# Kernel tuning notes

Measured on AMD Instinct MI355X. Metric: run time of the kernel, lower is better.

The kernel has to match this reference:

```python
import jax, jax.numpy as jnp
import numpy as np

D_MODEL = 1024
N_HEAD = 16
D_K = D_MODEL // N_HEAD
FFN = 4096
EPS = 1e-5


def layer_norm(x, g, b):
    mu = jnp.mean(x, axis=-1, keepdims=True)
    var = jnp.var(x, axis=-1, keepdims=True)
    return (x - mu) * jax.lax.rsqrt(var + EPS) * g + b


def setup_inputs() -> dict:
    key = jax.random.key(0)
    ks = jax.random.split(key, 16)
    B, L = 2, 2048
    s = 1.0 / np.sqrt(D_MODEL)
    inp = {
        "x": jax.random.normal(ks[0], (B, L, D_MODEL), dtype=jnp.float32),
        "mask": jnp.ones((B, 1, 1, L), dtype=jnp.int32),
        "ln1_g": jnp.ones((D_MODEL,), jnp.float32),
        "ln1_b": jnp.zeros((D_MODEL,), jnp.float32),
        "Wq": jax.random.normal(ks[1], (D_MODEL, D_MODEL), jnp.float32) * s,
        "bq": jnp.zeros((D_MODEL,), jnp.float32),
        "Wk": jax.random.normal(ks[2], (D_MODEL, D_MODEL), jnp.float32) * s,
        "bk": jnp.zeros((D_MODEL,), jnp.float32),
        "Wv": jax.random.normal(ks[3], (D_MODEL, D_MODEL), jnp.float32) * s,
        "bv": jnp.zeros((D_MODEL,), jnp.float32),
        "Wo": jax.random.normal(ks[4], (D_MODEL, D_MODEL), jnp.float32) * s,
        "bo": jnp.zeros((D_MODEL,), jnp.float32),
        "ln2_g": jnp.ones((D_MODEL,), jnp.float32),
        "ln2_b": jnp.zeros((D_MODEL,), jnp.float32),
        "W1": jax.random.normal(ks[5], (D_MODEL, FFN), jnp.float32) * s,
        "b1": jnp.zeros((FFN,), jnp.float32),
        "W2": jax.random.normal(ks[6], (FFN, D_MODEL), jnp.float32) * (1.0 / np.sqrt(FFN)),
        "b2": jnp.zeros((D_MODEL,), jnp.float32),
    }
    return inp


def reference(x, mask, ln1_g, ln1_b, Wq, bq, Wk, bk, Wv, bv, Wo, bo,
              ln2_g, ln2_b, W1, b1, W2, b2):
    B, L, _ = x.shape
    nx = layer_norm(x, ln1_g, ln1_b)
    # QKV projections, split heads -> [B, H, L, Dk]
    def proj(W, b):
        return (nx @ W + b).reshape(B, L, N_HEAD, D_K).transpose(0, 2, 1, 3)
    q, k, v = proj(Wq, bq), proj(Wk, bk), proj(Wv, bv)
    scores = jnp.einsum('bhqd,bhkd->bhqk', q, k) / np.sqrt(D_K)
    scores = jnp.where(mask.astype(bool), scores, -jnp.inf)
    attn = jax.nn.softmax(scores, axis=-1)
    out = jnp.einsum('bhqk,bhkd->bhqd', attn, v)
    out = out.transpose(0, 2, 1, 3).reshape(B, L, D_MODEL)
    out = out @ Wo + bo
    x = x + out  # residual (dropout p=0)
    nx = layer_norm(x, ln2_g, ln2_b)
    h = jax.nn.silu(nx @ W1 + b1)
    x = x + (h @ W2 + b2)
    return x
```

## Files before the change

### kernel.cpp

```cpp
#include <hip/hip_runtime.h>
#include <hip/hip_bf16.h>

#define D_MODEL 1024
#define N_HEAD  16
#define D_K     64
#define FFN_DIM 4096
#define B_SZ    2
#define L_SEQ   2048
#define ROWS    (B_SZ * L_SEQ)
#define PST     68

typedef float  floatx4 __attribute__((ext_vector_type(4)));
typedef short  shortx8 __attribute__((ext_vector_type(8)));

__device__ __forceinline__ unsigned short f2bf(float f) {
    unsigned int u = __float_as_uint(f);
    unsigned int rounding = 0x7fffu + ((u >> 16) & 1u);
    return (unsigned short)((u + rounding) >> 16);
}
__device__ __forceinline__ float bf2f(unsigned short u) {
    return __uint_as_float(((unsigned int)u) << 16);
}

__device__ __forceinline__ void glds16(const unsigned short* g, unsigned short* l) {
    __builtin_amdgcn_global_load_lds(
        (const __attribute__((address_space(1))) unsigned int*)g,
        (__attribute__((address_space(3))) unsigned int*)l, 16, 0, 0);
}

__global__ __launch_bounds__(256) void ln_kernel(const float* __restrict__ x,
                                                 const float* __restrict__ g,
                                                 const float* __restrict__ b,
                                                 unsigned short* __restrict__ out) {
    const int row = blockIdx.x;
    const int tid = threadIdx.x;
    const float* xr = x + (size_t)row * D_MODEL;
    float4 xv = *reinterpret_cast<const float4*>(&xr[tid * 4]);
    float v[4] = {xv.x, xv.y, xv.z, xv.w};
    float s = v[0] + v[1] + v[2] + v[3];
    float ss = v[0] * v[0] + v[1] * v[1] + v[2] * v[2] + v[3] * v[3];
    __shared__ float r1[256], r2[256];
    r1[tid] = s; r2[tid] = ss;
    __syncthreads();
    for (int off = 128; off > 0; off >>= 1) {
        if (tid < off) { r1[tid] += r1[tid + off]; r2[tid] += r2[tid + off]; }
        __syncthreads();
    }
    const float mean = r1[0] * (1.0f / D_MODEL);
    const float var  = r2[0] * (1.0f / D_MODEL) - mean * mean;
    const float inv  = rsqrtf(var + 1e-5f);
    unsigned short* orow = out + (size_t)row * D_MODEL;
    ushort4 o;
    o.x = f2bf((v[0] - mean) * inv * g[tid * 4 + 0] + b[tid * 4 + 0]);
    o.y = f2bf((v[1] - mean) * inv * g[tid * 4 + 1] + b[tid * 4 + 1]);
    o.z = f2bf((v[2] - mean) * inv * g[tid * 4 + 2] + b[tid * 4 + 2]);
    o.w = f2bf((v[3] - mean) * inv * g[tid * 4 + 3] + b[tid * 4 + 3]);
    *reinterpret_cast<ushort4*>(&orow[tid * 4]) = o;
}

__global__ __launch_bounds__(256) void transpose_cast(const float* __restrict__ W,
                                                      unsigned short* __restrict__ Wt,
                                                      int K, int N) {
    __shared__ unsigned short T[32][33];
    const int t = threadIdx.x;
    const int k0 = blockIdx.y * 32, n0 = blockIdx.x * 32;
    const int kr = t >> 3, nc = (t & 7) * 4;
    float4 w = *reinterpret_cast<const float4*>(&W[(size_t)(k0 + kr) * N + n0 + nc]);
    T[kr][nc + 0] = f2bf(w.x); T[kr][nc + 1] = f2bf(w.y);
    T[kr][nc + 2] = f2bf(w.z); T[kr][nc + 3] = f2bf(w.w);
    __syncthreads();
    const int nr = t >> 3, kc = (t & 7) * 4;
    ushort4 o;
    o.x = T[kc + 0][nr]; o.y = T[kc + 1][nr];
    o.z = T[kc + 2][nr]; o.w = T[kc + 3][nr];
    *reinterpret_cast<ushort4*>(&Wt[(size_t)(n0 + nr) * K + k0 + kc]) = o;
}

__global__ __launch_bounds__(256) void transpose_cast4(const float* s0, const float* s1,
                                                       const float* s2, const float* s3,
                                                       unsigned short* d0, unsigned short* d1,
                                                       unsigned short* d2, unsigned short* d3) {
    const int z = blockIdx.z;
    const float* W = (z == 0) ? s0 : (z == 1) ? s1 : (z == 2) ? s2 : s3;
    unsigned short* Wt = (z == 0) ? d0 : (z == 1) ? d1 : (z == 2) ? d2 : d3;
    __shared__ unsigned short T[32][33];
    const int t = threadIdx.x;
    const int k0 = blockIdx.y * 32, n0 = blockIdx.x * 32;
    const int kr = t >> 3, nc = (t & 7) * 4;
    float4 w = *reinterpret_cast<const float4*>(&W[(size_t)(k0 + kr) * D_MODEL + n0 + nc]);
    T[kr][nc + 0] = f2bf(w.x); T[kr][nc + 1] = f2bf(w.y);
    T[kr][nc + 2] = f2bf(w.z); T[kr][nc + 3] = f2bf(w.w);
    __syncthreads();
    const int nr = t >> 3, kc = (t & 7) * 4;
    ushort4 o;
    o.x = T[kc + 0][nr]; o.y = T[kc + 1][nr];
    o.z = T[kc + 2][nr]; o.w = T[kc + 3][nr];
    *reinterpret_cast<ushort4*>(&Wt[(size_t)(n0 + nr) * D_MODEL + k0 + kc]) = o;
}


template <int SILU, int HAS_RES, int OUT_BF16>
__global__ __launch_bounds__(256) void mfma_gemm(const unsigned short* __restrict__ A,
                                                 const unsigned short* __restrict__ Wt,
                                                 const float* __restrict__ bias,
                                                 const float* __restrict__ res,
                                                 void* __restrict__ outP,
                                                 int M, int N, int K) {
    __shared__ unsigned short As[128 * 32];
    __shared__ unsigned short Bs[128 * 32];
    const int tid  = threadIdx.x;
    const int lane = tid & 63;
    const int wave = tid >> 6;
    const int row0 = blockIdx.y * 128, col0 = blockIdx.x * 128;
    const int wr = (wave >> 1) * 64, wc = (wave & 1) * 64;

    floatx4 acc[4][4] = {};
    const int p0 = tid,       r0s = p0 >> 2, k0s = (((p0 & 3) - (r0s >> 1)) & 3) * 8;
    const int p1 = tid + 256, r1s = p1 >> 2, k1s = (((p1 & 3) - (r1s >> 1)) & 3) * 8;
    const int am = (lane & 15);

    int offA[4], offB[4];
#pragma unroll
    for (int i = 0; i < 4; ++i) {
        const int Ra = wr + i * 16 + am;
        offA[i] = Ra * 32 + (((lane >> 4) + (Ra >> 1)) & 3) * 8;
        const int Rb = wc + i * 16 + am;
        offB[i] = Rb * 32 + (((lane >> 4) + (Rb >> 1)) & 3) * 8;
    }

    for (int kt = 0; kt < K; kt += 32) {
        glds16(A  + (size_t)(row0 + r0s) * K + kt + k0s, &As[p0 * 8]);
        glds16(A  + (size_t)(row0 + r1s) * K + kt + k1s, &As[p1 * 8]);
        glds16(Wt + (size_t)(col0 + r0s) * K + kt + k0s, &Bs[p0 * 8]);
        glds16(Wt + (size_t)(col0 + r1s) * K + kt + k1s, &Bs[p1 * 8]);
        __syncthreads();
        shortx8 af[4], bf[4];
#pragma unroll
        for (int i = 0; i < 4; ++i)
            af[i] = *reinterpret_cast<const shortx8*>(&As[offA[i]]);
#pragma unroll
        for (int j = 0; j < 4; ++j)
            bf[j] = *reinterpret_cast<const shortx8*>(&Bs[offB[j]]);
#pragma unroll
        for (int i = 0; i < 4; ++i)
#pragma unroll
            for (int j = 0; j < 4; ++j)
                acc[i][j] = __builtin_amdgcn_mfma_f32_16x16x32_bf16(af[i], bf[j], acc[i][j], 0, 0, 0);
        __syncthreads();
    }

    const int cq = (lane >> 4) * 4;
    const int cn = lane & 15;
#pragma unroll
    for (int i = 0; i < 4; ++i) {
#pragma unroll
        for (int j = 0; j < 4; ++j) {
            const int n = col0 + wc + j * 16 + cn;
            const float bb = bias[n];
#pragma unroll
            for (int r = 0; r < 4; ++r) {
                const int m = row0 + wr + i * 16 + cq + r;
                float v = acc[i][j][r] + bb;
                if (SILU) v = v / (1.0f + __expf(-v));
                if (HAS_RES) v += res[(size_t)m * N + n];
                if (OUT_BF16) ((unsigned short*)outP)[(size_t)m * N + n] = f2bf(v);
                else          ((float*)outP)[(size_t)m * N + n] = v;
            }
        }
    }
}

__global__ __launch_bounds__(256) void mfma_gemm_qkv(const unsigned short* __restrict__ A,
                                                     const unsigned short* __restrict__ Wt,
                                                     const float* __restrict__ bq,
                                                     const float* __restrict__ bk,
                                                     const float* __restrict__ bv,
                                                     unsigned short* __restrict__ qb,
                                                     unsigned short* __restrict__ kb,
                                                     unsigned short* __restrict__ vtb) {
    const int K = D_MODEL, M = ROWS;
    __shared__ unsigned short As[128 * 32];
    __shared__ unsigned short Bs[128 * 32];
    const int tid  = threadIdx.x;
    const int lane = tid & 63;
    const int wave = tid >> 6;
    const int row0 = blockIdx.y * 128, col0 = blockIdx.x * 128;
    const int wr = (wave >> 1) * 64, wc = (wave & 1) * 64;

    floatx4 acc[4][4] = {};
    const int p0 = tid,       r0s = p0 >> 2, k0s = (((p0 & 3) - (r0s >> 1)) & 3) * 8;
    const int p1 = tid + 256, r1s = p1 >> 2, k1s = (((p1 & 3) - (r1s >> 1)) & 3) * 8;
    const int am = (lane & 15);

    int offA[4], offB[4];
#pragma unroll
    for (int i = 0; i < 4; ++i) {
        const int Ra = wr + i * 16 + am;
        offA[i] = Ra * 32 + (((lane >> 4) + (Ra >> 1)) & 3) * 8;
        const int Rb = wc + i * 16 + am;
        offB[i] = Rb * 32 + (((lane >> 4) + (Rb >> 1)) & 3) * 8;
    }

    for (int kt = 0; kt < K; kt += 32) {
        glds16(A  + (size_t)(row0 + r0s) * K + kt + k0s, &As[p0 * 8]);
        glds16(A  + (size_t)(row0 + r1s) * K + kt + k1s, &As[p1 * 8]);
        glds16(Wt + (size_t)(col0 + r0s) * K + kt + k0s, &Bs[p0 * 8]);
        glds16(Wt + (size_t)(col0 + r1s) * K + kt + k1s, &Bs[p1 * 8]);
        __syncthreads();
        shortx8 af[4], bf[4];
#pragma unroll
        for (int i = 0; i < 4; ++i)
            af[i] = *reinterpret_cast<const shortx8*>(&As[offA[i]]);
#pragma unroll
        for (int j = 0; j < 4; ++j)
            bf[j] = *reinterpret_cast<const shortx8*>(&Bs[offB[j]]);
#pragma unroll
        for (int i = 0; i < 4; ++i)
#pragma unroll
            for (int j = 0; j < 4; ++j)
                acc[i][j] = __builtin_amdgcn_mfma_f32_16x16x32_bf16(af[i], bf[j], acc[i][j], 0, 0, 0);
        __syncthreads();
    }

    const int cq = (lane >> 4) * 4;
    const int cn = lane & 15;
    const int sel = col0 >> 10;
    const int nbase = col0 & 1023;
    const float* bias = (sel == 0) ? bq : (sel == 1) ? bk : bv;
    const float scl = (sel == 0) ? 0.125f : 1.0f;
#pragma unroll
    for (int i = 0; i < 4; ++i) {
#pragma unroll
        for (int j = 0; j < 4; ++j) {
            const int n = nbase + wc + j * 16 + cn;
            const float bb = bias[n];
            if (sel == 2) {
                const int m0 = row0 + wr + i * 16 + cq;
                ushort4 o;
                o.x = f2bf(acc[i][j][0] + bb);
                o.y = f2bf(acc[i][j][1] + bb);
                o.z = f2bf(acc[i][j][2] + bb);
                o.w = f2bf(acc[i][j][3] + bb);
                *reinterpret_cast<ushort4*>(&vtb[(size_t)n * M + m0]) = o;
            } else {
                unsigned short* dst = (sel == 0) ? qb : kb;
#pragma unroll
                for (int r = 0; r < 4; ++r) {
                    const int m = row0 + wr + i * 16 + cq + r;
                    dst[(size_t)m * D_MODEL + n] = f2bf((acc[i][j][r] + bb) * scl);
                }
            }
        }
    }
}

__global__ __launch_bounds__(256) void mfma_gemm_splitk(const unsigned short* __restrict__ A,
                                                        const unsigned short* __restrict__ Wt,
                                                        unsigned short* __restrict__ parts,
                                                        int M, int N, int KS) {
    __shared__ unsigned short As[128 * 32];
    __shared__ unsigned short Bs[128 * 32];
    const int tid  = threadIdx.x;
    const int lane = tid & 63;
    const int wave = tid >> 6;
    const int row0 = blockIdx.y * 128, col0 = blockIdx.x * 128;
    const int wr = (wave >> 1) * 64, wc = (wave & 1) * 64;
    const int K = KS * gridDim.z;
    const int kbeg = blockIdx.z * KS;
    unsigned short* outp = parts + (size_t)blockIdx.z * M * N;

    floatx4 acc[4][4] = {};
    const int p0 = tid,       r0s = p0 >> 2, k0s = (((p0 & 3) - (r0s >> 1)) & 3) * 8;
    const int p1 = tid + 256, r1s = p1 >> 2, k1s = (((p1 & 3) - (r1s >> 1)) & 3) * 8;
    const int am = (lane & 15);

    int offA[4], offB[4];
#pragma unroll
    for (int i = 0; i < 4; ++i) {
        const int Ra = wr + i * 16 + am;
        offA[i] = Ra * 32 + (((lane >> 4) + (Ra >> 1)) & 3) * 8;
        const int Rb = wc + i * 16 + am;
        offB[i] = Rb * 32 + (((lane >> 4) + (Rb >> 1)) & 3) * 8;
    }

    for (int kt = kbeg; kt < kbeg + KS; kt += 32) {
        glds16(A  + (size_t)(row0 + r0s) * K + kt + k0s, &As[p0 * 8]);
        glds16(A  + (size_t)(row0 + r1s) * K + kt + k1s, &As[p1 * 8]);
        glds16(Wt + (size_t)(col0 + r0s) * K + kt + k0s, &Bs[p0 * 8]);
        glds16(Wt + (size_t)(col0 + r1s) * K + kt + k1s, &Bs[p1 * 8]);
        __syncthreads();
        shortx8 af[4], bf[4];
#pragma unroll
        for (int i = 0; i < 4; ++i)
            af[i] = *reinterpret_cast<const shortx8*>(&As[offA[i]]);
#pragma unroll
        for (int j = 0; j < 4; ++j)
            bf[j] = *reinterpret_cast<const shortx8*>(&Bs[offB[j]]);
#pragma unroll
        for (int i = 0; i < 4; ++i)
#pragma unroll
            for (int j = 0; j < 4; ++j)
                acc[i][j] = __builtin_amdgcn_mfma_f32_16x16x32_bf16(af[i], bf[j], acc[i][j], 0, 0, 0);
        __syncthreads();
    }

    const int cq = (lane >> 4) * 4;
    const int cn = lane & 15;
#pragma unroll
    for (int i = 0; i < 4; ++i)
#pragma unroll
        for (int j = 0; j < 4; ++j) {
            const int n = col0 + wc + j * 16 + cn;
#pragma unroll
            for (int r = 0; r < 4; ++r) {
                const int m = row0 + wr + i * 16 + cq + r;
                outp[(size_t)m * N + n] = f2bf(acc[i][j][r]);
            }
        }
}

__global__ __launch_bounds__(256) void combine_kernel(const unsigned short* __restrict__ p0,
                                                      const unsigned short* __restrict__ p1,
                                                      const float* __restrict__ bias,
                                                      const float* __restrict__ res,
                                                      float* __restrict__ out) {
    const size_t e0 = ((size_t)blockIdx.x * 256 + threadIdx.x) * 4;
    const int col = (int)(e0 & 1023);
    ushort4 a = *reinterpret_cast<const ushort4*>(&p0[e0]);
    ushort4 b = *reinterpret_cast<const ushort4*>(&p1[e0]);
    float4 r = *reinterpret_cast<const float4*>(&res[e0]);
    float4 o;
    o.x = bf2f(a.x) + bf2f(b.x) + bias[col + 0] + r.x;
    o.y = bf2f(a.y) + bf2f(b.y) + bias[col + 1] + r.y;
    o.z = bf2f(a.z) + bf2f(b.z) + bias[col + 2] + r.z;
    o.w = bf2f(a.w) + bf2f(b.w) + bias[col + 3] + r.w;
    *reinterpret_cast<float4*>(&out[e0]) = o;
}

__global__ __launch_bounds__(256) void attn_mfma(const unsigned short* __restrict__ Q,
                                                 const unsigned short* __restrict__ K,
                                                 const unsigned short* __restrict__ Vt,
                                                 const int* __restrict__ mask,
                                                 unsigned short* __restrict__ att) {
    const int tid  = threadIdx.x;
    const int lane = tid & 63;
    const int wave = tid >> 6;
    const int q0 = blockIdx.x * 64;
    const int h  = blockIdx.y;
    const int b  = blockIdx.z;

    __shared__ unsigned short Qs[64 * PST];
    __shared__ unsigned short Ks[64 * 64];
    __shared__ unsigned short Vs[64 * 64];
    __shared__ unsigned short Ps[64 * PST];
    __shared__ int mk[64];

    const int am = lane & 15;
    const int aq = (lane >> 4) * 8;
    const int cq = (lane >> 4) * 4;
    const int cn = lane & 15;

    for (int c = tid; c < 512; c += 256) {
        const int r = c >> 3, off = (c & 7) * 8;
        *reinterpret_cast<uint4*>(&Qs[r * PST + off]) =
            *reinterpret_cast<const uint4*>(&Q[(size_t)(b * L_SEQ + q0 + r) * D_MODEL + h * D_K + off]);
    }

    const int p0 = tid,       sr0 = p0 >> 3, sc0 = (((p0 & 7) - sr0) & 7) * 8;
    const int p1 = tid + 256, sr1 = p1 >> 3, sc1 = (((p1 & 7) - sr1) & 7) * 8;
    const unsigned short* K0 = K + (size_t)(b * L_SEQ + sr0) * D_MODEL + h * D_K + sc0;
    const unsigned short* K1 = K + (size_t)(b * L_SEQ + sr1) * D_MODEL + h * D_K + sc1;
    const unsigned short* V0 = Vt + (size_t)(h * D_K + sr0) * ROWS + b * L_SEQ + sc0;
    const unsigned short* V1 = Vt + (size_t)(h * D_K + sr1) * ROWS + b * L_SEQ + sc1;

    int offF[2][4];
#pragma unroll
    for (int kt = 0; kt < 2; ++kt)
#pragma unroll
        for (int t = 0; t < 4; ++t) {
            const int R = t * 16 + am;
            offF[kt][t] = R * 64 + (((kt * 4 + (lane >> 4)) + R) & 7) * 8;
        }

    __syncthreads();

    shortx8 aQ[2];
    aQ[0] = *reinterpret_cast<const shortx8*>(&Qs[(wave * 16 + am) * PST + aq]);
    aQ[1] = *reinterpret_cast<const shortx8*>(&Qs[(wave * 16 + am) * PST + 32 + aq]);

    floatx4 oacc[4] = {};
    float lsum[4] = {0.0f, 0.0f, 0.0f, 0.0f};

    for (int j0 = 0; j0 < L_SEQ; j0 += 64) {
        __syncthreads();
        glds16(K0 + (size_t)j0 * D_MODEL, &Ks[p0 * 8]);
        glds16(K1 + (size_t)j0 * D_MODEL, &Ks[p1 * 8]);
        glds16(V0 + j0, &Vs[p0 * 8]);
        glds16(V1 + j0, &Vs[p1 * 8]);
        if (tid < 64) mk[tid] = mask[b * L_SEQ + j0 + tid];
        __syncthreads();

        floatx4 sacc[4] = {};
#pragma unroll
        for (int kt = 0; kt < 2; ++kt)
#pragma unroll
            for (int jt = 0; jt < 4; ++jt) {
                shortx8 bK = *reinterpret_cast<const shortx8*>(&Ks[offF[kt][jt]]);
                sacc[jt] = __builtin_amdgcn_mfma_f32_16x16x32_bf16(aQ[kt], bK, sacc[jt], 0, 0, 0);
            }
#pragma unroll
        for (int jt = 0; jt < 4; ++jt) {
            const int mv = mk[jt * 16 + cn];
#pragma unroll
            for (int r = 0; r < 4; ++r) {
                float p = mv ? __expf(sacc[jt][r]) : 0.0f;
                lsum[r] += p;
                Ps[(wave * 16 + cq + r) * PST + jt * 16 + cn] =
                    (unsigned short)(__float_as_uint(p) >> 16);
            }
        }
#pragma unroll
        for (int kt = 0; kt < 2; ++kt) {
            shortx8 aP = *reinterpret_cast<const shortx8*>(&Ps[(wave * 16 + am) * PST + kt * 32 + aq]);
#pragma unroll
            for (int dt = 0; dt < 4; ++dt) {
                shortx8 bV = *reinterpret_cast<const shortx8*>(&Vs[offF[kt][dt]]);
                oacc[dt] = __builtin_amdgcn_mfma_f32_16x16x32_bf16(aP, bV, oacc[dt], 0, 0, 0);
            }
        }
    }

#pragma unroll
    for (int r = 0; r < 4; ++r) {
        float t = lsum[r];
        t += __shfl_xor(t, 1);
        t += __shfl_xor(t, 2);
        t += __shfl_xor(t, 4);
        t += __shfl_xor(t, 8);
        lsum[r] = 1.0f / t;
    }
#pragma unroll
    for (int dt = 0; dt < 4; ++dt)
#pragma unroll
        for (int r = 0; r < 4; ++r) {
            att[(size_t)(b * L_SEQ + q0 + wave * 16 + cq + r) * D_MODEL + h * D_K + dt * 16 + cn] =
                f2bf(oacc[dt][r] * lsum[r]);
        }
}

extern "C" void kernel_launch(void* const* d_in, const int* in_sizes, int n_in,
                              void* d_out, int out_size, void* d_ws, size_t ws_size,
                              hipStream_t stream) {
    const float* x     = (const float*)d_in[0];
    const int*   mask  = (const int*)d_in[1];
    const float* ln1_g = (const float*)d_in[2];
    const float* ln1_b = (const float*)d_in[3];
    const float* Wq    = (const float*)d_in[4];
    const float* bq    = (const float*)d_in[5];
    const float* Wk    = (const float*)d_in[6];
    const float* bk    = (const float*)d_in[7];
    const float* Wv    = (const float*)d_in[8];
    const float* bv    = (const float*)d_in[9];
    const float* Wo    = (const float*)d_in[10];
    const float* bo    = (const float*)d_in[11];
    const float* ln2_g = (const float*)d_in[12];
    const float* ln2_b = (const float*)d_in[13];
    const float* W1    = (const float*)d_in[14];
    const float* b1    = (const float*)d_in[15];
    const float* W2    = (const float*)d_in[16];
    const float* b2    = (const float*)d_in[17];
    float* out = (float*)d_out;

    float* ws = (float*)d_ws;
    const size_t SZ = (size_t)ROWS * D_MODEL;

    unsigned short* nx  = (unsigned short*)(ws + 0 * SZ);
    unsigned short* qb  = (unsigned short*)(ws + 1 * SZ);
    unsigned short* kb  = qb + SZ;
    unsigned short* vtb = (unsigned short*)(ws + 2 * SZ);
    unsigned short* attb = vtb + SZ;
    float* x1  = out;
    unsigned short* nx2 = nx;
    unsigned short* h = (unsigned short*)(ws + 2 * SZ);
    unsigned short* parts = (unsigned short*)(ws + 0 * SZ);

    unsigned short* WqkvT = (unsigned short*)(ws + 4 * SZ);
    unsigned short* WqT = WqkvT;
    unsigned short* WkT = WqkvT + (size_t)D_MODEL * D_MODEL;
    unsigned short* WvT = WkT + (size_t)D_MODEL * D_MODEL;
    unsigned short* WoT = WvT + (size_t)D_MODEL * D_MODEL;
    unsigned short* W1T = (unsigned short*)(ws + 1 * SZ);
    unsigned short* W2T = W1T + (size_t)D_MODEL * FFN_DIM;

    ln_kernel<<<ROWS, 256, 0, stream>>>(x, ln1_g, ln1_b, nx);

    transpose_cast4<<<dim3(32, 32, 4), 256, 0, stream>>>(Wq, Wk, Wv, Wo, WqT, WkT, WvT, WoT);

    mfma_gemm_qkv<<<dim3(3072 / 128, ROWS / 128), 256, 0, stream>>>(
        nx, WqkvT, bq, bk, bv, qb, kb, vtb);

    attn_mfma<<<dim3(L_SEQ / 64, N_HEAD, B_SZ), 256, 0, stream>>>(qb, kb, vtb, mask, attb);

    transpose_cast<<<dim3(FFN_DIM / 32, D_MODEL / 32), 256, 0, stream>>>(W1, W1T, D_MODEL, FFN_DIM);
    transpose_cast<<<dim3(D_MODEL / 32, FFN_DIM / 32), 256, 0, stream>>>(W2, W2T, FFN_DIM, D_MODEL);

    mfma_gemm<0, 1, 0><<<dim3(D_MODEL / 128, ROWS / 128), 256, 0, stream>>>(
        attb, WoT, bo, x, x1, ROWS, D_MODEL, D_MODEL);

    ln_kernel<<<ROWS, 256, 0, stream>>>(x1, ln2_g, ln2_b, nx2);

    mfma_gemm<1, 0, 1><<<dim3(FFN_DIM / 128, ROWS / 128), 256, 0, stream>>>(
        nx2, W1T, b1, nullptr, h, ROWS, FFN_DIM, D_MODEL);

    mfma_gemm_splitk<<<dim3(D_MODEL / 128, ROWS / 128, 2), 256, 0, stream>>>(
        h, W2T, parts, ROWS, D_MODEL, FFN_DIM / 2);
    combine_kernel<<<(ROWS * D_MODEL) / 1024, 256, 0, stream>>>(
        parts, parts + SZ, b2, x1, out);
}
```

Baseline: 413.4 us.

## Double-buffer K/V tiles in attention and fold log2e into Q scale

The attention loop now keeps two LDS buffers for K, V and the mask. The next 64-key tile is loaded while the current one is computed, removing the per-iteration load-then-sync stall. The Q projection scale now includes log2(e), so softmax can use exp2f directly instead of __expf, saving a multiply per score. This doubles K/V LDS usage, which may lower occupancy. Correctness depends on the async global-to-LDS loads having completed by the barrier.

```diff
diff --git a/kernel.cpp b/kernel.cpp
--- a/kernel.cpp
+++ b/kernel.cpp
@@ -227,7 +227,7 @@
     const int sel = col0 >> 10;
     const int nbase = col0 & 1023;
     const float* bias = (sel == 0) ? bq : (sel == 1) ? bk : bv;
-    const float scl = (sel == 0) ? 0.125f : 1.0f;
+    const float scl = (sel == 0) ? 0.18033688511157292f : 1.0f;
 #pragma unroll
     for (int i = 0; i < 4; ++i) {
 #pragma unroll
@@ -337,6 +337,49 @@
     *reinterpret_cast<float4*>(&out[e0]) = o;
 }
 
+
+#define ATTN_STAGE(BUF, J)                                                           \
+    do {                                                                             \
+        glds16(K0 + (size_t)(J) * D_MODEL, &Ks[BUF][p0 * 8]);                        \
+        glds16(K1 + (size_t)(J) * D_MODEL, &Ks[BUF][p1 * 8]);                        \
+        glds16(V0 + (J), &Vs[BUF][p0 * 8]);                                          \
+        glds16(V1 + (J), &Vs[BUF][p1 * 8]);                                          \
+        if (tid < 64) mk[BUF][tid] = mask[b * L_SEQ + (J) + tid];                    \
+    } while (0)
+
+#define ATTN_COMPUTE(BUF)                                                            \
+    do {                                                                             \
+        floatx4 sacc[4] = {};                                                        \
+        _Pragma("unroll")                                                            \
+        for (int kt = 0; kt < 2; ++kt) {                                             \
+            _Pragma("unroll")                                                        \
+            for (int jt = 0; jt < 4; ++jt) {                                         \
+                shortx8 bK = *reinterpret_cast<const shortx8*>(&Ks[BUF][offF[kt][jt]]); \
+                sacc[jt] = __builtin_amdgcn_mfma_f32_16x16x32_bf16(aQ[kt], bK, sacc[jt], 0, 0, 0); \
+            }                                                                        \
+        }                                                                            \
+        _Pragma("unroll")                                                            \
+        for (int jt = 0; jt < 4; ++jt) {                                             \
+            const int mv = mk[BUF][jt * 16 + cn];                                    \
+            _Pragma("unroll")                                                        \
+            for (int r = 0; r < 4; ++r) {                                            \
+                float p = mv ? exp2f(sacc[jt][r]) : 0.0f;                            \
+                lsum[r] += p;                                                        \
+                Ps[(wave * 16 + cq + r) * PST + jt * 16 + cn] =                      \
+                    (unsigned short)(__float_as_uint(p) >> 16);                      \
+            }                                                                        \
+        }                                                                            \
+        _Pragma("unroll")                                                            \
+        for (int kt = 0; kt < 2; ++kt) {                                             \
+            shortx8 aP = *reinterpret_cast<const shortx8*>(&Ps[(wave * 16 + am) * PST + kt * 32 + aq]); \
+            _Pragma("unroll")                                                        \
+            for (int dt = 0; dt < 4; ++dt) {                                         \
+                shortx8 bV = *reinterpret_cast<const shortx8*>(&Vs[BUF][offF[kt][dt]]); \
+                oacc[dt] = __builtin_amdgcn_mfma_f32_16x16x32_bf16(aP, bV, oacc[dt], 0, 0, 0); \
+            }                                                                        \
+        }                                                                            \
+    } while (0)
+
 __global__ __launch_bounds__(256) void attn_mfma(const unsigned short* __restrict__ Q,
                                                  const unsigned short* __restrict__ K,
                                                  const unsigned short* __restrict__ Vt,
@@ -350,10 +393,10 @@
     const int b  = blockIdx.z;
 
     __shared__ unsigned short Qs[64 * PST];
-    __shared__ unsigned short Ks[64 * 64];
-    __shared__ unsigned short Vs[64 * 64];
+    __shared__ unsigned short Ks[2][64 * 64];
+    __shared__ unsigned short Vs[2][64 * 64];
     __shared__ unsigned short Ps[64 * PST];
-    __shared__ int mk[64];
+    __shared__ int mk[2][64];
 
     const int am = lane & 15;
     const int aq = (lane >> 4) * 8;
@@ -382,52 +425,23 @@
             offF[kt][t] = R * 64 + (((kt * 4 + (lane >> 4)) + R) & 7) * 8;
         }
 
+    floatx4 oacc[4] = {};
+    float lsum[4] = {0.0f, 0.0f, 0.0f, 0.0f};
+
+    ATTN_STAGE(0, 0);
     __syncthreads();
 
     shortx8 aQ[2];
     aQ[0] = *reinterpret_cast<const shortx8*>(&Qs[(wave * 16 + am) * PST + aq]);
     aQ[1] = *reinterpret_cast<const shortx8*>(&Qs[(wave * 16 + am) * PST + 32 + aq]);
 
-    floatx4 oacc[4] = {};
-    float lsum[4] = {0.0f, 0.0f, 0.0f, 0.0f};
-
-    for (int j0 = 0; j0 < L_SEQ; j0 += 64) {
-        __syncthreads();
-        glds16(K0 + (size_t)j0 * D_MODEL, &Ks[p0 * 8]);
-        glds16(K1 + (size_t)j0 * D_MODEL, &Ks[p1 * 8]);
-        glds16(V0 + j0, &Vs[p0 * 8]);
-        glds16(V1 + j0, &Vs[p1 * 8]);
-        if (tid < 64) mk[tid] = mask[b * L_SEQ + j0 + tid];
-        __syncthreads();
-
-        floatx4 sacc[4] = {};
-#pragma unroll
-        for (int kt = 0; kt < 2; ++kt)
-#pragma unroll
-            for (int jt = 0; jt < 4; ++jt) {
-                shortx8 bK = *reinterpret_cast<const shortx8*>(&Ks[offF[kt][jt]]);
-                sacc[jt] = __builtin_amdgcn_mfma_f32_16x16x32_bf16(aQ[kt], bK, sacc[jt], 0, 0, 0);
-            }
-#pragma unroll
-        for (int jt = 0; jt < 4; ++jt) {
-            const int mv = mk[jt * 16 + cn];
-#pragma unroll
-            for (int r = 0; r < 4; ++r) {
-                float p = mv ? __expf(sacc[jt][r]) : 0.0f;
-                lsum[r] += p;
-                Ps[(wave * 16 + cq + r) * PST + jt * 16 + cn] =
-                    (unsigned short)(__float_as_uint(p) >> 16);
-            }
-        }
-#pragma unroll
-        for (int kt = 0; kt < 2; ++kt) {
-            shortx8 aP = *reinterpret_cast<const shortx8*>(&Ps[(wave * 16 + am) * PST + kt * 32 + aq]);
-#pragma unroll
-            for (int dt = 0; dt < 4; ++dt) {
-                shortx8 bV = *reinterpret_cast<const shortx8*>(&Vs[offF[kt][dt]]);
-                oacc[dt] = __builtin_amdgcn_mfma_f32_16x16x32_bf16(aP, bV, oacc[dt], 0, 0, 0);
-            }
-        }
+    for (int j0 = 0; j0 < L_SEQ; j0 += 128) {
+        ATTN_STAGE(1, j0 + 64);
+        ATTN_COMPUTE(0);
+        __syncthreads();
+        if (j0 + 128 < L_SEQ) ATTN_STAGE(0, j0 + 128);
+        ATTN_COMPUTE(1);
+        __syncthreads();
     }
 
 #pragma unroll
```

Measured after the change: 430.3 us. 1.04x slower.

## Register-prefetch next K/V tile in attention and fold log2e into Q scale

Applied to the files above, without the earlier changes.

The attention loop now loads the next K, V and mask tile from global memory into registers while the current tile's MFMAs run, then stores them to LDS at the top of the next iteration. This replaces the direct global-to-LDS copies that were issued and waited on between barriers. Separately, the Q projection scale now includes log2(e), so the softmax can call exp2f instead of __expf. The cost is extra registers for the prefetched data, which may reduce occupancy, and the barrier moves to the end of the loop.

```diff
diff --git a/kernel.cpp b/kernel.cpp
--- a/kernel.cpp
+++ b/kernel.cpp
@@ -227,7 +227,7 @@
     const int sel = col0 >> 10;
     const int nbase = col0 & 1023;
     const float* bias = (sel == 0) ? bq : (sel == 1) ? bk : bv;
-    const float scl = (sel == 0) ? 0.125f : 1.0f;
+    const float scl = (sel == 0) ? 0.18033688511157292f : 1.0f;
 #pragma unroll
     for (int i = 0; i < 4; ++i) {
 #pragma unroll
@@ -360,19 +360,26 @@
     const int cq = (lane >> 4) * 4;
     const int cn = lane & 15;
 
+    const int p0 = tid,       sr0 = p0 >> 3, sc0 = (((p0 & 7) - sr0) & 7) * 8;
+    const int p1 = tid + 256, sr1 = p1 >> 3, sc1 = (((p1 & 7) - sr1) & 7) * 8;
+    const unsigned short* pK0 = K + (size_t)(b * L_SEQ + sr0) * D_MODEL + h * D_K + sc0;
+    const unsigned short* pK1 = K + (size_t)(b * L_SEQ + sr1) * D_MODEL + h * D_K + sc1;
+    const unsigned short* pV0 = Vt + (size_t)(h * D_K + sr0) * ROWS + b * L_SEQ + sc0;
+    const unsigned short* pV1 = Vt + (size_t)(h * D_K + sr1) * ROWS + b * L_SEQ + sc1;
+    const int* pM = mask + b * L_SEQ;
+
+    uint4 kA = *reinterpret_cast<const uint4*>(pK0);
+    uint4 kB = *reinterpret_cast<const uint4*>(pK1);
+    uint4 vA = *reinterpret_cast<const uint4*>(pV0);
+    uint4 vB = *reinterpret_cast<const uint4*>(pV1);
+    int   mr = (tid < 64) ? pM[tid] : 0;
+
     for (int c = tid; c < 512; c += 256) {
         const int r = c >> 3, off = (c & 7) * 8;
         *reinterpret_cast<uint4*>(&Qs[r * PST + off]) =
             *reinterpret_cast<const uint4*>(&Q[(size_t)(b * L_SEQ + q0 + r) * D_MODEL + h * D_K + off]);
     }
 
-    const int p0 = tid,       sr0 = p0 >> 3, sc0 = (((p0 & 7) - sr0) & 7) * 8;
-    const int p1 = tid + 256, sr1 = p1 >> 3, sc1 = (((p1 & 7) - sr1) & 7) * 8;
-    const unsigned short* K0 = K + (size_t)(b * L_SEQ + sr0) * D_MODEL + h * D_K + sc0;
-    const unsigned short* K1 = K + (size_t)(b * L_SEQ + sr1) * D_MODEL + h * D_K + sc1;
-    const unsigned short* V0 = Vt + (size_t)(h * D_K + sr0) * ROWS + b * L_SEQ + sc0;
-    const unsigned short* V1 = Vt + (size_t)(h * D_K + sr1) * ROWS + b * L_SEQ + sc1;
-
     int offF[2][4];
 #pragma unroll
     for (int kt = 0; kt < 2; ++kt)
@@ -392,13 +399,22 @@
     float lsum[4] = {0.0f, 0.0f, 0.0f, 0.0f};
 
     for (int j0 = 0; j0 < L_SEQ; j0 += 64) {
-        __syncthreads();
-        glds16(K0 + (size_t)j0 * D_MODEL, &Ks[p0 * 8]);
-        glds16(K1 + (size_t)j0 * D_MODEL, &Ks[p1 * 8]);
-        glds16(V0 + j0, &Vs[p0 * 8]);
-        glds16(V1 + j0, &Vs[p1 * 8]);
-        if (tid < 64) mk[tid] = mask[b * L_SEQ + j0 + tid];
-        __syncthreads();
+        *reinterpret_cast<uint4*>(&Ks[p0 * 8]) = kA;
+        *reinterpret_cast<uint4*>(&Ks[p1 * 8]) = kB;
+        *reinterpret_cast<uint4*>(&Vs[p0 * 8]) = vA;
+        *reinterpret_cast<uint4*>(&Vs[p1 * 8]) = vB;
+        if (tid < 64) mk[tid] = mr;
+        __syncthreads();
+
+        if (j0 + 64 < L_SEQ) {
+            pK0 += 64 * D_MODEL; pK1 += 64 * D_MODEL;
+            pV0 += 64;           pV1 += 64;
+            kA = *reinterpret_cast<const uint4*>(pK0);
+            kB = *reinterpret_cast<const uint4*>(pK1);
+            vA = *reinterpret_cast<const uint4*>(pV0);
+            vB = *reinterpret_cast<const uint4*>(pV1);
+            mr = (tid < 64) ? pM[j0 + 64 + tid] : 0;
+        }
 
         floatx4 sacc[4] = {};
 #pragma unroll
@@ -413,7 +429,7 @@
             const int mv = mk[jt * 16 + cn];
 #pragma unroll
             for (int r = 0; r < 4; ++r) {
-                float p = mv ? __expf(sacc[jt][r]) : 0.0f;
+                float p = mv ? exp2f(sacc[jt][r]) : 0.0f;
                 lsum[r] += p;
                 Ps[(wave * 16 + cq + r) * PST + jt * 16 + cn] =
                     (unsigned short)(__float_as_uint(p) >> 16);
@@ -428,6 +444,7 @@
                 oacc[dt] = __builtin_amdgcn_mfma_f32_16x16x32_bf16(aP, bV, oacc[dt], 0, 0, 0);
             }
         }
+        __syncthreads();
     }
 
 #pragma unroll
```

Result: no change. 417.3 us (+0.9%).

## Split-K the output projection, deepen W2 split-K to four, fold log2e into Q scale

Applied to the files above, without the earlier changes.

The Wo projection now uses the split-K GEMM with two K-halves plus a combine kernel that adds bias and residual, instead of the full-K fused GEMM. The W2 GEMM moves from two to four K-splits with a new four-way combine kernel. The Q scale absorbs log2(e) so attention can use exp2f instead of __expf, and the workspace is re-laid out in MB offsets so the extra partial buffers fit. The goal is more blocks in flight for the N=1024 GEMMs, which otherwise launch only 256 tiles, in exchange for extra partial-sum traffic and bf16 rounding of the partials.

```diff
diff --git a/kernel.cpp b/kernel.cpp
--- a/kernel.cpp
+++ b/kernel.cpp
@@ -227,7 +227,7 @@
     const int sel = col0 >> 10;
     const int nbase = col0 & 1023;
     const float* bias = (sel == 0) ? bq : (sel == 1) ? bk : bv;
-    const float scl = (sel == 0) ? 0.125f : 1.0f;
+    const float scl = (sel == 0) ? 0.18033688511157292f : 1.0f;
 #pragma unroll
     for (int i = 0; i < 4; ++i) {
 #pragma unroll
@@ -337,6 +337,28 @@
     *reinterpret_cast<float4*>(&out[e0]) = o;
 }
 
+__global__ __launch_bounds__(256) void combine4_kernel(const unsigned short* __restrict__ p0,
+                                                       const unsigned short* __restrict__ p1,
+                                                       const unsigned short* __restrict__ p2,
+                                                       const unsigned short* __restrict__ p3,
+                                                       const float* __restrict__ bias,
+                                                       const float* __restrict__ res,
+                                                       float* __restrict__ out) {
+    const size_t e0 = ((size_t)blockIdx.x * 256 + threadIdx.x) * 4;
+    const int col = (int)(e0 & 1023);
+    ushort4 a = *reinterpret_cast<const ushort4*>(&p0[e0]);
+    ushort4 b = *reinterpret_cast<const ushort4*>(&p1[e0]);
+    ushort4 c = *reinterpret_cast<const ushort4*>(&p2[e0]);
+    ushort4 d = *reinterpret_cast<const ushort4*>(&p3[e0]);
+    float4 r = *reinterpret_cast<const float4*>(&res[e0]);
+    float4 o;
+    o.x = (bf2f(a.x) + bf2f(b.x)) + (bf2f(c.x) + bf2f(d.x)) + bias[col + 0] + r.x;
+    o.y = (bf2f(a.y) + bf2f(b.y)) + (bf2f(c.y) + bf2f(d.y)) + bias[col + 1] + r.y;
+    o.z = (bf2f(a.z) + bf2f(b.z)) + (bf2f(c.z) + bf2f(d.z)) + bias[col + 2] + r.z;
+    o.w = (bf2f(a.w) + bf2f(b.w)) + (bf2f(c.w) + bf2f(d.w)) + bias[col + 3] + r.w;
+    *reinterpret_cast<float4*>(&out[e0]) = o;
+}
+
 __global__ __launch_bounds__(256) void attn_mfma(const unsigned short* __restrict__ Q,
                                                  const unsigned short* __restrict__ K,
                                                  const unsigned short* __restrict__ Vt,
@@ -413,7 +435,7 @@
             const int mv = mk[jt * 16 + cn];
 #pragma unroll
             for (int r = 0; r < 4; ++r) {
-                float p = mv ? __expf(sacc[jt][r]) : 0.0f;
+                float p = mv ? exp2f(sacc[jt][r]) : 0.0f;
                 lsum[r] += p;
                 Ps[(wave * 16 + cq + r) * PST + jt * 16 + cn] =
                     (unsigned short)(__float_as_uint(p) >> 16);
@@ -471,26 +493,26 @@
     const float* b2    = (const float*)d_in[17];
     float* out = (float*)d_out;
 
-    float* ws = (float*)d_ws;
+    char* base = (char*)d_ws;
+    const size_t MB = 1024 * 1024;
     const size_t SZ = (size_t)ROWS * D_MODEL;
 
-    unsigned short* nx  = (unsigned short*)(ws + 0 * SZ);
-    unsigned short* qb  = (unsigned short*)(ws + 1 * SZ);
-    unsigned short* kb  = qb + SZ;
-    unsigned short* vtb = (unsigned short*)(ws + 2 * SZ);
-    unsigned short* attb = vtb + SZ;
-    float* x1  = out;
-    unsigned short* nx2 = nx;
-    unsigned short* h = (unsigned short*)(ws + 2 * SZ);
-    unsigned short* parts = (unsigned short*)(ws + 0 * SZ);
-
-    unsigned short* WqkvT = (unsigned short*)(ws + 4 * SZ);
-    unsigned short* WqT = WqkvT;
-    unsigned short* WkT = WqkvT + (size_t)D_MODEL * D_MODEL;
-    unsigned short* WvT = WkT + (size_t)D_MODEL * D_MODEL;
-    unsigned short* WoT = WvT + (size_t)D_MODEL * D_MODEL;
-    unsigned short* W1T = (unsigned short*)(ws + 1 * SZ);
-    unsigned short* W2T = W1T + (size_t)D_MODEL * FFN_DIM;
+    unsigned short* nx    = (unsigned short*)(base + 0);
+    unsigned short* qb    = (unsigned short*)(base + 16 * MB);
+    unsigned short* kb    = (unsigned short*)(base + 24 * MB);
+    unsigned short* vtb   = (unsigned short*)(base + 32 * MB);
+    unsigned short* attb  = (unsigned short*)(base + 40 * MB);
+    unsigned short* parts = (unsigned short*)(base + 0);
+    unsigned short* h     = (unsigned short*)(base + 32 * MB);
+    unsigned short* WqkvT = (unsigned short*)(base + 64 * MB);
+    unsigned short* WqT   = WqkvT;
+    unsigned short* WkT   = WqkvT + (size_t)D_MODEL * D_MODEL;
+    unsigned short* WvT   = WkT + (size_t)D_MODEL * D_MODEL;
+    unsigned short* WoT   = (unsigned short*)(base + 70 * MB);
+    unsigned short* W1T   = (unsigned short*)(base + 16 * MB);
+    unsigned short* W2T   = (unsigned short*)(base + 64 * MB);
+    unsigned short* nx2   = nx;
+    float* x1 = out;
 
     ln_kernel<<<ROWS, 256, 0, stream>>>(x, ln1_g, ln1_b, nx);
 
@@ -502,18 +524,21 @@
     attn_mfma<<<dim3(L_SEQ / 64, N_HEAD, B_SZ), 256, 0, stream>>>(qb, kb, vtb, mask, attb);
 
     transpose_cast<<<dim3(FFN_DIM / 32, D_MODEL / 32), 256, 0, stream>>>(W1, W1T, D_MODEL, FFN_DIM);
+
+    mfma_gemm_splitk<<<dim3(D_MODEL / 128, ROWS / 128, 2), 256, 0, stream>>>(
+        attb, WoT, parts, ROWS, D_MODEL, D_MODEL / 2);
+    combine_kernel<<<(ROWS * D_MODEL) / 1024, 256, 0, stream>>>(
+        parts, parts + SZ, bo, x, x1);
+
     transpose_cast<<<dim3(D_MODEL / 32, FFN_DIM / 32), 256, 0, stream>>>(W2, W2T, FFN_DIM, D_MODEL);
-
-    mfma_gemm<0, 1, 0><<<dim3(D_MODEL / 128, ROWS / 128), 256, 0, stream>>>(
-        attb, WoT, bo, x, x1, ROWS, D_MODEL, D_MODEL);
 
     ln_kernel<<<ROWS, 256, 0, stream>>>(x1, ln2_g, ln2_b, nx2);
 
     mfma_gemm<1, 0, 1><<<dim3(FFN_DIM / 128, ROWS / 128), 256, 0, stream>>>(
         nx2, W1T, b1, nullptr, h, ROWS, FFN_DIM, D_MODEL);
 
-    mfma_gemm_splitk<<<dim3(D_MODEL / 128, ROWS / 128, 2), 256, 0, stream>>>(
-        h, W2T, parts, ROWS, D_MODEL, FFN_DIM / 2);
-    combine_kernel<<<(ROWS * D_MODEL) / 1024, 256, 0, stream>>>(
-        parts, parts + SZ, b2, x1, out);
-}
+    mfma_gemm_splitk<<<dim3(D_MODEL / 128, ROWS / 128, 4), 256, 0, stream>>>(
+        h, W2T, parts, ROWS, D_MODEL, FFN_DIM / 4);
+    combine4_kernel<<<(ROWS * D_MODEL) / 1024, 256, 0, stream>>>(
+        parts, parts + SZ, parts + 2 * SZ, parts + 3 * SZ, b2, x1, out);
+}
```

After: 428.0 us. +3.5%, slower.
